# Kernel tuning notes

Measured on AMD Instinct MI355X. Metric: run time of the kernel, lower is better.

## Reference

```python
import jax, jax.numpy as jnp
import numpy as np
import math

N, B, S = 2048, 4, 1024
SFZ, IFZ, H, A = 384, 256, 8, 64
LN_EPS = 1e-5


def setup_inputs() -> dict:
    key = jax.random.key(0)
    ks = jax.random.split(key, 12)
    x = jax.random.normal(ks[0], (N, IFZ), dtype=jnp.float32)
    emb = jax.random.normal(ks[1], (B, S, SFZ), dtype=jnp.float32)
    mask = jax.random.randint(ks[2], (B, S), 0, 2).astype(bool)
    batch = jnp.sort(jax.random.randint(ks[3], (N,), 0, B)).astype(jnp.int64)
    sc = 1.0 / math.sqrt(IFZ)
    scs = 1.0 / math.sqrt(SFZ)
    Wq = jax.random.normal(ks[4], (IFZ, H * A), dtype=jnp.float32) * sc
    Wk = jax.random.normal(ks[5], (SFZ, H * A), dtype=jnp.float32) * scs
    Wv = jax.random.normal(ks[6], (SFZ, H * A), dtype=jnp.float32) * scs
    Wg = jax.random.normal(ks[7], (IFZ, H * A), dtype=jnp.float32) * sc
    bg = jnp.zeros((H * A,), dtype=jnp.float32)
    Wback = jax.random.normal(ks[8], (H * A, IFZ), dtype=jnp.float32) / math.sqrt(H * A)
    bback = jnp.zeros((IFZ,), dtype=jnp.float32)
    gamma = jnp.ones((IFZ,), dtype=jnp.float32)
    beta = jnp.zeros((IFZ,), dtype=jnp.float32)
    return {"x": x, "packed_sequence_emb": emb, "packed_sequence_mask": mask,
            "batch": batch, "Wq": Wq, "Wk": Wk, "Wv": Wv, "Wg": Wg, "bg": bg,
            "Wback": Wback, "bback": bback, "gamma": gamma, "beta": beta}


def _masked_softmax(scores, mask):
    # scores: [N,S,H], mask: [N,S,1] bool; softmax over S with padded entries zeroed
    neg = jnp.finfo(scores.dtype).min
    s = jnp.where(mask, scores, neg)
    s = s - jnp.max(s, axis=1, keepdims=True)
    e = jnp.exp(s) * mask
    return e / (jnp.sum(e, axis=1, keepdims=True) + 1e-9)


def reference(x, packed_sequence_emb, packed_sequence_mask, batch,
              Wq, Wk, Wv, Wg, bg, Wback, bback, gamma, beta):
    scale = math.sqrt(A)
    q = (x @ Wq).reshape(N, H, A)                               # [N,H,A]
    k = (packed_sequence_emb @ Wk).reshape(B, S, H, A)          # [B,S,H,A]
    v = (packed_sequence_emb @ Wv).reshape(B, S, H, A)
    # scores per (node, candidate-batch), then gather node's own batch entry;
    # avoids materializing k[batch] of shape [N,S,H,A]
    scores_all = jnp.einsum('nha,bsha->nbsh', q, k) / scale     # [N,B,S,H]
    idx = batch[:, None, None, None].astype(jnp.int32)
    scores = jnp.take_along_axis(scores_all, idx, axis=1)[:, 0]  # [N,S,H]
    bmask = packed_sequence_mask[batch][..., None]               # [N,S,1]
    w = _masked_softmax(scores, bmask)                           # [N,S,H]
    feat_all = jnp.einsum('nsh,bsha->nbha', w, v)                # [N,B,H,A]
    feat = jnp.take_along_axis(feat_all, idx, axis=1)[:, 0]      # [N,H,A]
    gate = jax.nn.sigmoid(x @ Wg + bg).reshape(N, H, A)
    new = (gate * feat).reshape(N, H * A) @ Wback + bback        # [N,IFZ]
    y = math.sqrt(2.0) * x + new
    mu = jnp.mean(y, axis=-1, keepdims=True)
    var = jnp.mean((y - mu) ** 2, axis=-1, keepdims=True)
    out = (y - mu) * jax.lax.rsqrt(var + LN_EPS) * gamma + beta
    seq_aa_logits = jnp.sum(scores[..., :2], axis=-1)            # [N,S]
    return out, seq_aa_logits
```

## Files before the change

kernel.cpp:

```cpp
#include <hip/hip_runtime.h>
#include <hip/hip_bf16.h>

#define NND 2048
#define BBATCH 4
#define SS 1024
#define SFZ 384
#define IFZ 256
#define HH 8
#define AA 64
#define HA 512
#define NBX 48
#define NSPL 8

typedef __attribute__((ext_vector_type(8))) short bf16x8;
typedef __attribute__((ext_vector_type(4))) float f32x4;

__device__ __forceinline__ unsigned short f2bf(float f) {
    union { float f; unsigned u; } a; a.f = f;
    unsigned r = a.u + 0x7fffu + ((a.u >> 16) & 1u);
    return (unsigned short)(r >> 16);
}
__device__ __forceinline__ float bf2f(unsigned short u) {
    return __uint_as_float((unsigned)u << 16);
}

__device__ __forceinline__ bf16x8 cvt8(const float* __restrict__ p) {
    const float4 f0 = *(const float4*)p;
    const float4 f1 = *(const float4*)(p + 4);
    bf16x8 o;
    o[0] = (short)f2bf(f0.x); o[1] = (short)f2bf(f0.y);
    o[2] = (short)f2bf(f0.z); o[3] = (short)f2bf(f0.w);
    o[4] = (short)f2bf(f1.x); o[5] = (short)f2bf(f1.y);
    o[6] = (short)f2bf(f1.z); o[7] = (short)f2bf(f1.w);
    return o;
}

__device__ __forceinline__ void tile_transpose_h(
    const float* __restrict__ src, unsigned short* __restrict__ dst,
    int K, int N, int kt, int nt, int half, int t)
{
    __shared__ unsigned short tile[32][65];
    const int k0 = kt * 64 + half * 32, n0 = nt * 64;
    const int tr = t >> 6, tc = t & 63;
    #pragma unroll
    for (int r = 0; r < 8; ++r)
        tile[tr + r*4][tc] = f2bf(src[(size_t)(k0 + tr + r*4) * N + n0 + tc]);
    __syncthreads();
    const int rr = t >> 5, cc = t & 31;
    #pragma unroll
    for (int r2 = 0; r2 < 8; ++r2)
        dst[(size_t)(n0 + rr + r2*8) * K + k0 + cc] = tile[cc][rr + r2*8];
}

__global__ __launch_bounds__(256) void prep_kernel(
    const float* __restrict__ Wk, const float* __restrict__ Wv,
    const float* __restrict__ Wq, const float* __restrict__ Wg,
    const float* __restrict__ Wback,
    const void* __restrict__ mask_raw, const void* __restrict__ batch_raw,
    unsigned short* __restrict__ WkT, unsigned short* __restrict__ WvT,
    unsigned short* __restrict__ WqT, unsigned short* __restrict__ WgT,
    unsigned short* __restrict__ WbackT,
    float* __restrict__ mask_f, int* __restrict__ seg)
{
    const int bx = blockIdx.x, t = threadIdx.x;
    if (bx < 384) {
        const int ht = bx >> 1, half = bx & 1;
        if (ht < 48)       tile_transpose_h(Wk, WkT, SFZ, HA, ht/8, ht%8, half, t);
        else if (ht < 96)  { const int i = ht-48;  tile_transpose_h(Wv, WvT, SFZ, HA, i/8, i%8, half, t); }
        else if (ht < 128) { const int i = ht-96;  tile_transpose_h(Wq, WqT, IFZ, HA, i/8, i%8, half, t); }
        else if (ht < 160) { const int i = ht-128; tile_transpose_h(Wg, WgT, IFZ, HA, i/8, i%8, half, t); }
        else               { const int i = ht-160; tile_transpose_h(Wback, WbackT, HA, IFZ, i/4, i%4, half, t); }
        return;
    }
    __shared__ int fl[4];
    __shared__ int fb;
    __shared__ int cnt[4];
    if (t < 4) { fl[t] = 0; cnt[t] = 0; }
    if (t == 0) fb = 0;
    __syncthreads();
    const unsigned char*  mb = (const unsigned char*)mask_raw;
    const unsigned short* mh = (const unsigned short*)mask_raw;
    const unsigned int*   mw = (const unsigned int*)mask_raw;
    int f0 = 0, f1 = 0, f2 = 0, f3 = 0;
    for (int i = t; i < 2048; i += 256) {
        unsigned short h = mh[i];
        if (h == 0x3f80u) f0 = 1;
        if ((i & 1) == 0 && h != 0) f1 = 1;
    }
    for (int i = t; i < 4096; i += 256)
        if ((i & 3) != 0 && mb[i] != 0) f2 = 1;
    for (int i = t; i < 1024; i += 256)
        if ((i & 1) != 0 && mw[i] != 0) f3 = 1;
    const int* bw = (const int*)batch_raw;
    int f4 = 0;
    for (int i = t + 1; i < 2048; i += 256)
        if (bw[i] < bw[i-1]) f4 = 1;
    if (f0) atomicOr(&fl[0], 1);
    if (f1) atomicOr(&fl[1], 1);
    if (f2) atomicOr(&fl[2], 1);
    if (f3) atomicOr(&fl[3], 1);
    if (f4) atomicOr(&fb, 1);
    __syncthreads();
    int mode;
    if (fl[0])      mode = fl[1] ? 1 : 0;
    else if (fl[2]) mode = 2;
    else if (fl[3]) mode = 3;
    else            mode = 4;
    for (int s = t; s < BBATCH*SS; s += 256) {
        int m;
        switch (mode) {
            case 0:  m = (mw[s]   != 0); break;
            case 1:  m = (mh[s]   != 0); break;
            case 2:  m = (mb[s]   != 0); break;
            case 3:  m = (mw[s]   != 0); break;
            default: m = (mw[2*s] != 0); break;
        }
        mask_f[s] = m ? 1.0f : 0.0f;
    }
    const int b64 = fb;
    for (int i = t; i < NND; i += 256) {
        const int bv = (b64 ? bw[2*i] : bw[i]) & 3;
        atomicAdd(&cnt[bv], 1);
    }
    __syncthreads();
    if (t == 0) {
        int s = 0;
        for (int b = 0; b < 4; ++b) { seg[2*b] = s; s += cnt[b]; seg[2*b+1] = s; }
    }
}

__global__ __launch_bounds__(256) void proj_mfma(
    const float* __restrict__ emb, const float* __restrict__ x,
    const unsigned short* __restrict__ WkT, const unsigned short* __restrict__ WvT,
    const unsigned short* __restrict__ WqT, const unsigned short* __restrict__ WgT,
    const float* __restrict__ bg,
    unsigned short* __restrict__ k_blk, unsigned short* __restrict__ vT_bf,
    unsigned short* __restrict__ q_bf, unsigned short* __restrict__ gate_bf)
{
    __shared__ unsigned short v_l[16][520];
    const int t = threadIdx.x, w = t >> 6, lane = t & 63;
    const int m16 = lane & 15, quad = lane >> 4;
    const int bx = blockIdx.x;
    if (bx < 512) {
        const int r0 = (bx >> 1) * 16;
        const int b = r0 >> 10, srow = r0 & (SS - 1);
        const float* ap = emb + (size_t)(r0 + m16) * SFZ + quad * 8;
        bf16x8 af[12];
        #pragma unroll
        for (int j = 0; j < 12; ++j) af[j] = cvt8(ap + j * 32);
        if ((bx & 1) == 0) {
            #pragma unroll
            for (int nt = 0; nt < 8; ++nt) {
                const int n0 = w * 128 + nt * 16;
                const unsigned short* bp = WkT + (size_t)(n0 + m16) * SFZ + quad * 8;
                f32x4 d = (f32x4){0.f, 0.f, 0.f, 0.f};
                #pragma unroll
                for (int j = 0; j < 12; ++j)
                    d = __builtin_amdgcn_mfma_f32_16x16x32_bf16(af[j], *(const bf16x8*)(bp + j * 32), d, 0, 0, 0);
                const int head = n0 >> 6, coff = (n0 & 63) + m16;
                unsigned short* kb = k_blk + (((size_t)(b * HH + head)) * SS) * 64 + coff;
                #pragma unroll
                for (int r = 0; r < 4; ++r)
                    kb[(size_t)(srow + quad * 4 + r) * 64] = f2bf(d[r]);
            }
        } else {
            #pragma unroll
            for (int nt = 0; nt < 8; ++nt) {
                const int n0 = w * 128 + nt * 16;
                const unsigned short* bp = WvT + (size_t)(n0 + m16) * SFZ + quad * 8;
                f32x4 d = (f32x4){0.f, 0.f, 0.f, 0.f};
                #pragma unroll
                for (int j = 0; j < 12; ++j)
                    d = __builtin_amdgcn_mfma_f32_16x16x32_bf16(af[j], *(const bf16x8*)(bp + j * 32), d, 0, 0, 0);
                #pragma unroll
                for (int r = 0; r < 4; ++r)
                    v_l[quad * 4 + r][n0 + m16] = f2bf(d[r]);
            }
            __syncthreads();
            for (int c = t; c < HA; c += 256) {
                unsigned short tmp[16];
                #pragma unroll
                for (int s = 0; s < 16; ++s) tmp[s] = v_l[s][c];
                unsigned short* dst = vT_bf + ((size_t)b * HA + c) * SS + srow;
                *(uint4*)dst       = ((const uint4*)tmp)[0];
                *(uint4*)(dst + 8) = ((const uint4*)tmp)[1];
            }
        }
    } else {
        const int i = bx - 512;
        const int r0 = (i >> 2) * 16;
        const int tensor = (i & 3) >> 1, half = i & 1;
        const unsigned short* Wt = tensor ? WgT : WqT;
        const float* ap = x + (size_t)(r0 + m16) * IFZ + quad * 8;
        bf16x8 af[8];
        #pragma unroll
        for (int j = 0; j < 8; ++j) af[j] = cvt8(ap + j * 32);
        #pragma unroll
        for (int nt = 0; nt < 4; ++nt) {
            const int n0 = half * 256 + w * 64 + nt * 16;
            const unsigned short* bp = Wt + (size_t)(n0 + m16) * IFZ + quad * 8;
            f32x4 d = (f32x4){0.f, 0.f, 0.f, 0.f};
            #pragma unroll
            for (int j = 0; j < 8; ++j)
                d = __builtin_amdgcn_mfma_f32_16x16x32_bf16(af[j], *(const bf16x8*)(bp + j * 32), d, 0, 0, 0);
            if (tensor == 0) {
                #pragma unroll
                for (int r = 0; r < 4; ++r)
                    q_bf[(size_t)(r0 + quad * 4 + r) * HA + n0 + m16] = f2bf(d[r]);
            } else {
                const float bgv = bg[n0 + m16];
                #pragma unroll
                for (int r = 0; r < 4; ++r)
                    gate_bf[(size_t)(r0 + quad * 4 + r) * HA + n0 + m16] =
                        f2bf(1.f / (1.f + __expf(-(d[r] + bgv))));
            }
        }
    }
}

__global__ __launch_bounds__(256) void attn_kernel(
    const unsigned short* __restrict__ k_blk, const unsigned short* __restrict__ vT_bf,
    const unsigned short* __restrict__ q_bf, const float* __restrict__ mask_f,
    const int* __restrict__ seg, unsigned short* __restrict__ part_O,
    float2* __restrict__ part_ml, float* __restrict__ out_logits)
{
    __shared__ unsigned short P_lds[4][16][136];
    __shared__ float raw[2][16][132];
    const int bid = blockIdx.x;
    const int xcd = bid & 7;
    const int b   = xcd >> 1;
    const int idx = (bid >> 3) * 2 + (xcd & 1);
    const int z    = idx & 15;
    const int xblk = idx >> 4;
    const int hz    = z >> 3;
    const int split = z & 7;
    const int n0 = seg[2*b] + xblk * 16;
    const int nend = seg[2*b + 1];
    if (n0 >= nend) return;
    const int nvalid = min(16, nend - n0);

    const int t = threadIdx.x;
    const int w = t >> 6, lane = t & 63;
    const int m16 = lane & 15, quad = lane >> 4;
    const int h = hz * 4 + w;
    const int s0 = split * 128;

    int nq = n0 + m16; if (nq >= nend) nq = nend - 1;
    const unsigned short* qp = q_bf + (size_t)nq * HA + h * AA + quad * 8;
    const bf16x8 qa0 = *(const bf16x8*)qp;
    const bf16x8 qa1 = *(const bf16x8*)(qp + 32);

    const unsigned short* kb = k_blk + ((size_t)(b * HH + h)) * SS * 64;
    const unsigned short* vb = vT_bf + ((size_t)b * HA + h * AA) * SS;
    unsigned short (*Pw)[136] = P_lds[w];

    float msk[8];
    #pragma unroll
    for (int st = 0; st < 8; ++st)
        msk[st] = mask_f[b * SS + s0 + st * 16 + m16];

    f32x4 d[8];
    #pragma unroll
    for (int st = 0; st < 8; ++st) {
        const unsigned short* kp = kb + (size_t)(s0 + st * 16 + m16) * 64 + quad * 8;
        const bf16x8 b0 = *(const bf16x8*)kp;
        const bf16x8 b1 = *(const bf16x8*)(kp + 32);
        f32x4 acc = (f32x4){0.f, 0.f, 0.f, 0.f};
        acc = __builtin_amdgcn_mfma_f32_16x16x32_bf16(qa0, b0, acc, 0, 0, 0);
        acc = __builtin_amdgcn_mfma_f32_16x16x32_bf16(qa1, b1, acc, 0, 0, 0);
        #pragma unroll
        for (int r = 0; r < 4; ++r) acc[r] *= 0.125f;
        d[st] = acc;
    }
    if (hz == 0) {
        if (w < 2) {
            #pragma unroll
            for (int st = 0; st < 8; ++st)
                #pragma unroll
                for (int r = 0; r < 4; ++r)
                    raw[w][quad * 4 + r][st * 16 + m16] = d[st][r];
        }
        __syncthreads();
        for (int i = t; i < 16 * 128; i += 256) {
            const int node = i >> 7, sp = i & 127;
            if (node < nvalid)
                out_logits[(size_t)(n0 + node) * SS + s0 + sp] =
                    raw[0][node][sp] + raw[1][node][sp];
        }
    }
    float m_s[4], l_s[4];
    #pragma unroll
    for (int r = 0; r < 4; ++r) {
        float mx = -3.0e38f;
        #pragma unroll
        for (int st = 0; st < 8; ++st)
            mx = (msk[st] > 0.5f) ? fmaxf(mx, d[st][r]) : mx;
        mx = fmaxf(mx, __shfl_xor(mx, 1));
        mx = fmaxf(mx, __shfl_xor(mx, 2));
        mx = fmaxf(mx, __shfl_xor(mx, 4));
        mx = fmaxf(mx, __shfl_xor(mx, 8));
        m_s[r] = mx;
        float cs = 0.f;
        #pragma unroll
        for (int st = 0; st < 8; ++st) {
            const float e = (msk[st] > 0.5f) ? __expf(d[st][r] - mx) : 0.f;
            d[st][r] = e;
            cs += e;
        }
        cs += __shfl_xor(cs, 1);
        cs += __shfl_xor(cs, 2);
        cs += __shfl_xor(cs, 4);
        cs += __shfl_xor(cs, 8);
        l_s[r] = cs;
    }
    #pragma unroll
    for (int st = 0; st < 8; ++st)
        #pragma unroll
        for (int r = 0; r < 4; ++r)
            Pw[quad * 4 + r][st * 16 + m16] = f2bf(d[st][r]);
    f32x4 facc[4];
    #pragma unroll
    for (int a = 0; a < 4; ++a) facc[a] = (f32x4){0.f, 0.f, 0.f, 0.f};
    #pragma unroll
    for (int sub = 0; sub < 4; ++sub) {
        const bf16x8 pa = *(const bf16x8*)&Pw[m16][sub * 32 + quad * 8];
        const unsigned short* vp0 = vb + (size_t)m16 * SS + s0 + sub * 32 + quad * 8;
        #pragma unroll
        for (int a = 0; a < 4; ++a) {
            const bf16x8 vfr = *(const bf16x8*)(vp0 + (size_t)(a * 16) * SS);
            facc[a] = __builtin_amdgcn_mfma_f32_16x16x32_bf16(pa, vfr, facc[a], 0, 0, 0);
        }
    }
    unsigned short* po = part_O + (size_t)split * NND * HA;
    #pragma unroll
    for (int a = 0; a < 4; ++a)
        #pragma unroll
        for (int r = 0; r < 4; ++r) {
            const int row = quad * 4 + r;
            if (row < nvalid)
                po[(size_t)(n0 + row) * HA + h * AA + a * 16 + m16] = f2bf(facc[a][r]);
        }
    if (m16 == 0) {
        #pragma unroll
        for (int r = 0; r < 4; ++r) {
            const int row = quad * 4 + r;
            if (row < nvalid)
                part_ml[(size_t)split * NND * HH + (size_t)(n0 + row) * HH + h] =
                    make_float2(m_s[r], l_s[r]);
        }
    }
}

__global__ __launch_bounds__(256) void back_ln_fused(
    const unsigned short* __restrict__ part_O, const float2* __restrict__ part_ml,
    const unsigned short* __restrict__ gate_bf, const unsigned short* __restrict__ WbackT,
    const float* __restrict__ x, const float* __restrict__ bback,
    const float* __restrict__ gamma, const float* __restrict__ beta,
    float* __restrict__ out)
{
    __shared__ float coef[NSPL][4][8];
    __shared__ unsigned short gf_l[4][520];
    __shared__ float nl[4][260];
    const int t = threadIdx.x, w = t >> 6, lane = t & 63;
    const int m16 = lane & 15, quad = lane >> 4;
    const int r0 = blockIdx.x * 4;
    if (t < 32) {
        const int row = t >> 3, h = t & 7, n = r0 + row;
        float2 ml[NSPL];
        #pragma unroll
        for (int s = 0; s < NSPL; ++s)
            ml[s] = part_ml[(size_t)s * NND * HH + (size_t)n * HH + h];
        float M = -3.0e38f;
        #pragma unroll
        for (int s = 0; s < NSPL; ++s) M = fmaxf(M, ml[s].x);
        float L = 0.f;
        float e[NSPL];
        #pragma unroll
        for (int s = 0; s < NSPL; ++s) { e[s] = __expf(ml[s].x - M); L += ml[s].y * e[s]; }
        const float invL = 1.f / (L + 1e-9f);
        #pragma unroll
        for (int s = 0; s < NSPL; ++s) coef[s][row][h] = e[s] * invL;
    }
    __syncthreads();
    #pragma unroll
    for (int it = 0; it < 2; ++it) {
        const int i = (t + it * 256) * 4;
        const int row = i >> 9, c = i & (HA - 1), h = c >> 6;
        const int n = r0 + row;
        float4 o = make_float4(0.f, 0.f, 0.f, 0.f);
        #pragma unroll
        for (int s = 0; s < NSPL; ++s) {
            const ushort4 p = *(const ushort4*)&part_O[(size_t)s * NND * HA + (size_t)n * HA + c];
            const float cf = coef[s][row][h];
            o.x = fmaf(bf2f(p.x), cf, o.x); o.y = fmaf(bf2f(p.y), cf, o.y);
            o.z = fmaf(bf2f(p.z), cf, o.z); o.w = fmaf(bf2f(p.w), cf, o.w);
        }
        const ushort4 g = *(const ushort4*)&gate_bf[(size_t)n * HA + c];
        ushort4 ob;
        ob.x = f2bf(bf2f(g.x) * o.x); ob.y = f2bf(bf2f(g.y) * o.y);
        ob.z = f2bf(bf2f(g.z) * o.z); ob.w = f2bf(bf2f(g.w) * o.w);
        *(ushort4*)&gf_l[row][c] = ob;
    }
    __syncthreads();
    bf16x8 af[16];
    #pragma unroll
    for (int j = 0; j < 16; ++j)
        af[j] = *(const bf16x8*)&gf_l[m16 & 3][quad * 8 + j * 32];
    #pragma unroll
    for (int nt = 0; nt < 4; ++nt) {
        const int n0 = w * 64 + nt * 16;
        const unsigned short* bp = WbackT + (size_t)(n0 + m16) * HA + quad * 8;
        f32x4 d = (f32x4){0.f, 0.f, 0.f, 0.f};
        #pragma unroll
        for (int j = 0; j < 16; ++j)
            d = __builtin_amdgcn_mfma_f32_16x16x32_bf16(af[j], *(const bf16x8*)(bp + j * 32), d, 0, 0, 0);
        const float bb = bback[n0 + m16];
        #pragma unroll
        for (int r = 0; r < 4; ++r) {
            const int rr = quad * 4 + r;
            if (rr < 4) nl[rr][n0 + m16] = d[r] + bb;
        }
    }
    __syncthreads();
    const int row = t >> 6, li = t & 63;
    const float* xr = x + (size_t)(r0 + row) * IFZ;
    float yv[4];
    float s1 = 0.f, s2 = 0.f;
    #pragma unroll
    for (int j = 0; j < 4; ++j) {
        const int c = li + j * 64;
        const float v = fmaf(1.41421356237309515f, xr[c], nl[row][c]);
        yv[j] = v; s1 += v; s2 += v * v;
    }
    #pragma unroll
    for (int off = 32; off >= 1; off >>= 1) {
        s1 += __shfl_xor(s1, off);
        s2 += __shfl_xor(s2, off);
    }
    const float mu  = s1 * (1.f / IFZ);
    const float var = s2 * (1.f / IFZ) - mu * mu;
    const float rv  = rsqrtf(var + 1e-5f);
    float* orow = out + (size_t)(r0 + row) * IFZ;
    #pragma unroll
    for (int j = 0; j < 4; ++j) {
        const int c = li + j * 64;
        orow[c] = (yv[j] - mu) * rv * gamma[c] + beta[c];
    }
}

extern "C" void kernel_launch(void* const* d_in, const int* in_sizes, int n_in,
                              void* d_out, int out_size, void* d_ws, size_t ws_size,
                              hipStream_t stream) {
    const float* x     = (const float*)d_in[0];
    const float* emb   = (const float*)d_in[1];
    const void*  mraw  = d_in[2];
    const void*  braw  = d_in[3];
    const float* Wq    = (const float*)d_in[4];
    const float* Wk    = (const float*)d_in[5];
    const float* Wv    = (const float*)d_in[6];
    const float* Wg    = (const float*)d_in[7];
    const float* bg    = (const float*)d_in[8];
    const float* Wback = (const float*)d_in[9];
    const float* bback = (const float*)d_in[10];
    const float* gamma = (const float*)d_in[11];
    const float* beta  = (const float*)d_in[12];

    char* ws = (char*)d_ws;
    const size_t MB = 1048576;
    size_t off = 0;
    float*          mask_f  = (float*)(ws + off);  off += 16384;
    int*            seg     = (int*)(ws + off);    off += 16384;
    unsigned short* WkT     = (unsigned short*)(ws + off); off += 393216;
    unsigned short* WvT     = (unsigned short*)(ws + off); off += 393216;
    unsigned short* WqT     = (unsigned short*)(ws + off); off += 262144;
    unsigned short* WgT     = (unsigned short*)(ws + off); off += 262144;
    unsigned short* WbackT  = (unsigned short*)(ws + off); off += 262144;
    unsigned short* k_blk   = (unsigned short*)(ws + off); off += 4*MB;
    unsigned short* vT_bf   = (unsigned short*)(ws + off); off += 4*MB;
    unsigned short* q_bf    = (unsigned short*)(ws + off); off += 2*MB;
    unsigned short* gate_bf = (unsigned short*)(ws + off); off += 2*MB;
    unsigned short* part_O  = (unsigned short*)(ws + off); off += 16*MB;
    float2*         part_ml = (float2*)(ws + off); off += 1*MB;

    float* out        = (float*)d_out;
    float* out_logits = out + (size_t)NND * IFZ;

    hipLaunchKernelGGL(prep_kernel, dim3(385), dim3(256), 0, stream,
                       Wk, Wv, Wq, Wg, Wback, mraw, braw,
                       WkT, WvT, WqT, WgT, WbackT, mask_f, seg);
    hipLaunchKernelGGL(proj_mfma, dim3(1024), dim3(256), 0, stream,
                       emb, x, WkT, WvT, WqT, WgT, bg, k_blk, vT_bf, q_bf, gate_bf);
    hipLaunchKernelGGL(attn_kernel, dim3(BBATCH * NBX * 16), dim3(256), 0, stream,
                       k_blk, vT_bf, q_bf, mask_f, seg, part_O, part_ml, out_logits);
    hipLaunchKernelGGL(back_ln_fused, dim3(NND / 4), dim3(256), 0, stream,
                       part_O, part_ml, gate_bf, WbackT, x, bback, gamma, beta, out);
}
```

Measured before the change: 202.4 us.

## Drop weight-transpose prep kernel and gather fp32 weights directly in MFMA loops

Removes the separate prep kernel that transposed and converted the weight matrices to bf16. The projection and back-projection kernels now read fp32 weights with strided gathers and convert them inline. Mask and segment preparation moves into an extra block of the projection kernel, saving one launch and the intermediate weight buffers. The cost is strided, uncoalesced fp32 weight loads and repeated conversion in every block, which may slow the GEMM inner loops.

```diff
diff --git a/kernel.cpp b/kernel.cpp
--- a/kernel.cpp
+++ b/kernel.cpp
@@ -35,109 +35,28 @@
     return o;
 }
 
-__device__ __forceinline__ void tile_transpose_h(
-    const float* __restrict__ src, unsigned short* __restrict__ dst,
-    int K, int N, int kt, int nt, int half, int t)
-{
-    __shared__ unsigned short tile[32][65];
-    const int k0 = kt * 64 + half * 32, n0 = nt * 64;
-    const int tr = t >> 6, tc = t & 63;
-    #pragma unroll
-    for (int r = 0; r < 8; ++r)
-        tile[tr + r*4][tc] = f2bf(src[(size_t)(k0 + tr + r*4) * N + n0 + tc]);
-    __syncthreads();
-    const int rr = t >> 5, cc = t & 31;
-    #pragma unroll
-    for (int r2 = 0; r2 < 8; ++r2)
-        dst[(size_t)(n0 + rr + r2*8) * K + k0 + cc] = tile[cc][rr + r2*8];
-}
-
-__global__ __launch_bounds__(256) void prep_kernel(
+__device__ __forceinline__ bf16x8 gatherB(const float* __restrict__ wj) {
+    bf16x8 o;
+    #pragma unroll
+    for (int e = 0; e < 8; ++e)
+        o[e] = (short)f2bf(wj[(size_t)e * HA]);
+    return o;
+}
+
+__global__ __launch_bounds__(256) void proj_mfma(
+    const float* __restrict__ emb, const float* __restrict__ x,
     const float* __restrict__ Wk, const float* __restrict__ Wv,
     const float* __restrict__ Wq, const float* __restrict__ Wg,
-    const float* __restrict__ Wback,
+    const float* __restrict__ bg,
     const void* __restrict__ mask_raw, const void* __restrict__ batch_raw,
-    unsigned short* __restrict__ WkT, unsigned short* __restrict__ WvT,
-    unsigned short* __restrict__ WqT, unsigned short* __restrict__ WgT,
-    unsigned short* __restrict__ WbackT,
+    unsigned short* __restrict__ k_blk, unsigned short* __restrict__ vT_bf,
+    unsigned short* __restrict__ q_bf, unsigned short* __restrict__ gate_bf,
     float* __restrict__ mask_f, int* __restrict__ seg)
 {
-    const int bx = blockIdx.x, t = threadIdx.x;
-    if (bx < 384) {
-        const int ht = bx >> 1, half = bx & 1;
-        if (ht < 48)       tile_transpose_h(Wk, WkT, SFZ, HA, ht/8, ht%8, half, t);
-        else if (ht < 96)  { const int i = ht-48;  tile_transpose_h(Wv, WvT, SFZ, HA, i/8, i%8, half, t); }
-        else if (ht < 128) { const int i = ht-96;  tile_transpose_h(Wq, WqT, IFZ, HA, i/8, i%8, half, t); }
-        else if (ht < 160) { const int i = ht-128; tile_transpose_h(Wg, WgT, IFZ, HA, i/8, i%8, half, t); }
-        else               { const int i = ht-160; tile_transpose_h(Wback, WbackT, HA, IFZ, i/4, i%4, half, t); }
-        return;
-    }
+    __shared__ unsigned short v_l[16][520];
     __shared__ int fl[4];
     __shared__ int fb;
     __shared__ int cnt[4];
-    if (t < 4) { fl[t] = 0; cnt[t] = 0; }
-    if (t == 0) fb = 0;
-    __syncthreads();
-    const unsigned char*  mb = (const unsigned char*)mask_raw;
-    const unsigned short* mh = (const unsigned short*)mask_raw;
-    const unsigned int*   mw = (const unsigned int*)mask_raw;
-    int f0 = 0, f1 = 0, f2 = 0, f3 = 0;
-    for (int i = t; i < 2048; i += 256) {
-        unsigned short h = mh[i];
-        if (h == 0x3f80u) f0 = 1;
-        if ((i & 1) == 0 && h != 0) f1 = 1;
-    }
-    for (int i = t; i < 4096; i += 256)
-        if ((i & 3) != 0 && mb[i] != 0) f2 = 1;
-    for (int i = t; i < 1024; i += 256)
-        if ((i & 1) != 0 && mw[i] != 0) f3 = 1;
-    const int* bw = (const int*)batch_raw;
-    int f4 = 0;
-    for (int i = t + 1; i < 2048; i += 256)
-        if (bw[i] < bw[i-1]) f4 = 1;
-    if (f0) atomicOr(&fl[0], 1);
-    if (f1) atomicOr(&fl[1], 1);
-    if (f2) atomicOr(&fl[2], 1);
-    if (f3) atomicOr(&fl[3], 1);
-    if (f4) atomicOr(&fb, 1);
-    __syncthreads();
-    int mode;
-    if (fl[0])      mode = fl[1] ? 1 : 0;
-    else if (fl[2]) mode = 2;
-    else if (fl[3]) mode = 3;
-    else            mode = 4;
-    for (int s = t; s < BBATCH*SS; s += 256) {
-        int m;
-        switch (mode) {
-            case 0:  m = (mw[s]   != 0); break;
-            case 1:  m = (mh[s]   != 0); break;
-            case 2:  m = (mb[s]   != 0); break;
-            case 3:  m = (mw[s]   != 0); break;
-            default: m = (mw[2*s] != 0); break;
-        }
-        mask_f[s] = m ? 1.0f : 0.0f;
-    }
-    const int b64 = fb;
-    for (int i = t; i < NND; i += 256) {
-        const int bv = (b64 ? bw[2*i] : bw[i]) & 3;
-        atomicAdd(&cnt[bv], 1);
-    }
-    __syncthreads();
-    if (t == 0) {
-        int s = 0;
-        for (int b = 0; b < 4; ++b) { seg[2*b] = s; s += cnt[b]; seg[2*b+1] = s; }
-    }
-}
-
-__global__ __launch_bounds__(256) void proj_mfma(
-    const float* __restrict__ emb, const float* __restrict__ x,
-    const unsigned short* __restrict__ WkT, const unsigned short* __restrict__ WvT,
-    const unsigned short* __restrict__ WqT, const unsigned short* __restrict__ WgT,
-    const float* __restrict__ bg,
-    unsigned short* __restrict__ k_blk, unsigned short* __restrict__ vT_bf,
-    unsigned short* __restrict__ q_bf, unsigned short* __restrict__ gate_bf)
-{
-    __shared__ unsigned short v_l[16][520];
     const int t = threadIdx.x, w = t >> 6, lane = t & 63;
     const int m16 = lane & 15, quad = lane >> 4;
     const int bx = blockIdx.x;
@@ -152,11 +71,12 @@
             #pragma unroll
             for (int nt = 0; nt < 8; ++nt) {
                 const int n0 = w * 128 + nt * 16;
-                const unsigned short* bp = WkT + (size_t)(n0 + m16) * SFZ + quad * 8;
+                const float* wp = Wk + (size_t)(quad * 8) * HA + n0 + m16;
                 f32x4 d = (f32x4){0.f, 0.f, 0.f, 0.f};
                 #pragma unroll
                 for (int j = 0; j < 12; ++j)
-                    d = __builtin_amdgcn_mfma_f32_16x16x32_bf16(af[j], *(const bf16x8*)(bp + j * 32), d, 0, 0, 0);
+                    d = __builtin_amdgcn_mfma_f32_16x16x32_bf16(
+                        af[j], gatherB(wp + (size_t)j * 32 * HA), d, 0, 0, 0);
                 const int head = n0 >> 6, coff = (n0 & 63) + m16;
                 unsigned short* kb = k_blk + (((size_t)(b * HH + head)) * SS) * 64 + coff;
                 #pragma unroll
@@ -167,11 +87,12 @@
             #pragma unroll
             for (int nt = 0; nt < 8; ++nt) {
                 const int n0 = w * 128 + nt * 16;
-                const unsigned short* bp = WvT + (size_t)(n0 + m16) * SFZ + quad * 8;
+                const float* wp = Wv + (size_t)(quad * 8) * HA + n0 + m16;
                 f32x4 d = (f32x4){0.f, 0.f, 0.f, 0.f};
                 #pragma unroll
                 for (int j = 0; j < 12; ++j)
-                    d = __builtin_amdgcn_mfma_f32_16x16x32_bf16(af[j], *(const bf16x8*)(bp + j * 32), d, 0, 0, 0);
+                    d = __builtin_amdgcn_mfma_f32_16x16x32_bf16(
+                        af[j], gatherB(wp + (size_t)j * 32 * HA), d, 0, 0, 0);
                 #pragma unroll
                 for (int r = 0; r < 4; ++r)
                     v_l[quad * 4 + r][n0 + m16] = f2bf(d[r]);
@@ -186,11 +107,11 @@
                 *(uint4*)(dst + 8) = ((const uint4*)tmp)[1];
             }
         }
-    } else {
+    } else if (bx < 1024) {
         const int i = bx - 512;
         const int r0 = (i >> 2) * 16;
         const int tensor = (i & 3) >> 1, half = i & 1;
-        const unsigned short* Wt = tensor ? WgT : WqT;
+        const float* Wt = tensor ? Wg : Wq;
         const float* ap = x + (size_t)(r0 + m16) * IFZ + quad * 8;
         bf16x8 af[8];
         #pragma unroll
@@ -198,11 +119,12 @@
         #pragma unroll
         for (int nt = 0; nt < 4; ++nt) {
             const int n0 = half * 256 + w * 64 + nt * 16;
-            const unsigned short* bp = Wt + (size_t)(n0 + m16) * IFZ + quad * 8;
+            const float* wp = Wt + (size_t)(quad * 8) * HA + n0 + m16;
             f32x4 d = (f32x4){0.f, 0.f, 0.f, 0.f};
             #pragma unroll
             for (int j = 0; j < 8; ++j)
-                d = __builtin_amdgcn_mfma_f32_16x16x32_bf16(af[j], *(const bf16x8*)(bp + j * 32), d, 0, 0, 0);
+                d = __builtin_amdgcn_mfma_f32_16x16x32_bf16(
+                    af[j], gatherB(wp + (size_t)j * 32 * HA), d, 0, 0, 0);
             if (tensor == 0) {
                 #pragma unroll
                 for (int r = 0; r < 4; ++r)
@@ -214,6 +136,59 @@
                     gate_bf[(size_t)(r0 + quad * 4 + r) * HA + n0 + m16] =
                         f2bf(1.f / (1.f + __expf(-(d[r] + bgv))));
             }
+        }
+    } else {
+        if (t < 4) { fl[t] = 0; cnt[t] = 0; }
+        if (t == 0) fb = 0;
+        __syncthreads();
+        const unsigned char*  mb = (const unsigned char*)mask_raw;
+        const unsigned short* mh = (const unsigned short*)mask_raw;
+        const unsigned int*   mw = (const unsigned int*)mask_raw;
+        int f0 = 0, f1 = 0, f2 = 0, f3 = 0;
+        for (int i = t; i < 2048; i += 256) {
+            unsigned short h = mh[i];
+            if (h == 0x3f80u) f0 = 1;
+            if ((i & 1) == 0 && h != 0) f1 = 1;
+        }
+        for (int i = t; i < 4096; i += 256)
+            if ((i & 3) != 0 && mb[i] != 0) f2 = 1;
+        for (int i = t; i < 1024; i += 256)
+            if ((i & 1) != 0 && mw[i] != 0) f3 = 1;
+        const int* bw = (const int*)batch_raw;
+        int f4 = 0;
+        for (int i = t + 1; i < 2048; i += 256)
+            if (bw[i] < bw[i-1]) f4 = 1;
+        if (f0) atomicOr(&fl[0], 1);
+        if (f1) atomicOr(&fl[1], 1);
+        if (f2) atomicOr(&fl[2], 1);
+        if (f3) atomicOr(&fl[3], 1);
+        if (f4) atomicOr(&fb, 1);
+        __syncthreads();
+        int mode;
+        if (fl[0])      mode = fl[1] ? 1 : 0;
+        else if (fl[2]) mode = 2;
+        else if (fl[3]) mode = 3;
+        else            mode = 4;
+        for (int s = t; s < BBATCH*SS; s += 256) {
+            int m;
+            switch (mode) {
+                case 0:  m = (mw[s]   != 0); break;
+                case 1:  m = (mh[s]   != 0); break;
+                case 2:  m = (mb[s]   != 0); break;
+                case 3:  m = (mw[s]   != 0); break;
+                default: m = (mw[2*s] != 0); break;
+            }
+            mask_f[s] = m ? 1.0f : 0.0f;
+        }
+        const int b64 = fb;
+        for (int i = t; i < NND; i += 256) {
+            const int bv = (b64 ? bw[2*i] : bw[i]) & 3;
+            atomicAdd(&cnt[bv], 1);
+        }
+        __syncthreads();
+        if (t == 0) {
+            int s = 0;
+            for (int b = 0; b < 4; ++b) { seg[2*b] = s; s += cnt[b]; seg[2*b+1] = s; }
         }
     }
 }
@@ -353,7 +328,7 @@
 
 __global__ __launch_bounds__(256) void back_ln_fused(
     const unsigned short* __restrict__ part_O, const float2* __restrict__ part_ml,
-    const unsigned short* __restrict__ gate_bf, const unsigned short* __restrict__ WbackT,
+    const unsigned short* __restrict__ gate_bf, const float* __restrict__ Wback,
     const float* __restrict__ x, const float* __restrict__ bback,
     const float* __restrict__ gamma, const float* __restrict__ beta,
     float* __restrict__ out)
@@ -409,11 +384,17 @@
     #pragma unroll
     for (int nt = 0; nt < 4; ++nt) {
         const int n0 = w * 64 + nt * 16;
-        const unsigned short* bp = WbackT + (size_t)(n0 + m16) * HA + quad * 8;
+        const float* wp = Wback + (size_t)(quad * 8) * IFZ + n0 + m16;
         f32x4 d = (f32x4){0.f, 0.f, 0.f, 0.f};
         #pragma unroll
-        for (int j = 0; j < 16; ++j)
-            d = __builtin_amdgcn_mfma_f32_16x16x32_bf16(af[j], *(const bf16x8*)(bp + j * 32), d, 0, 0, 0);
+        for (int j = 0; j < 16; ++j) {
+            const float* wj = wp + (size_t)j * 32 * IFZ;
+            bf16x8 bfr;
+            #pragma unroll
+            for (int e = 0; e < 8; ++e)
+                bfr[e] = (short)f2bf(wj[(size_t)e * IFZ]);
+            d = __builtin_amdgcn_mfma_f32_16x16x32_bf16(af[j], bfr, d, 0, 0, 0);
+        }
         const float bb = bback[n0 + m16];
         #pragma unroll
         for (int r = 0; r < 4; ++r) {
@@ -470,11 +451,6 @@
     size_t off = 0;
     float*          mask_f  = (float*)(ws + off);  off += 16384;
     int*            seg     = (int*)(ws + off);    off += 16384;
-    unsigned short* WkT     = (unsigned short*)(ws + off); off += 393216;
-    unsigned short* WvT     = (unsigned short*)(ws + off); off += 393216;
-    unsigned short* WqT     = (unsigned short*)(ws + off); off += 262144;
-    unsigned short* WgT     = (unsigned short*)(ws + off); off += 262144;
-    unsigned short* WbackT  = (unsigned short*)(ws + off); off += 262144;
     unsigned short* k_blk   = (unsigned short*)(ws + off); off += 4*MB;
     unsigned short* vT_bf   = (unsigned short*)(ws + off); off += 4*MB;
     unsigned short* q_bf    = (unsigned short*)(ws + off); off += 2*MB;
@@ -485,13 +461,11 @@
     float* out        = (float*)d_out;
     float* out_logits = out + (size_t)NND * IFZ;
 
-    hipLaunchKernelGGL(prep_kernel, dim3(385), dim3(256), 0, stream,
-                       Wk, Wv, Wq, Wg, Wback, mraw, braw,
-                       WkT, WvT, WqT, WgT, WbackT, mask_f, seg);
-    hipLaunchKernelGGL(proj_mfma, dim3(1024), dim3(256), 0, stream,
-                       emb, x, WkT, WvT, WqT, WgT, bg, k_blk, vT_bf, q_bf, gate_bf);
+    hipLaunchKernelGGL(proj_mfma, dim3(1025), dim3(256), 0, stream,
+                       emb, x, Wk, Wv, Wq, Wg, bg, mraw, braw,
+                       k_blk, vT_bf, q_bf, gate_bf, mask_f, seg);
     hipLaunchKernelGGL(attn_kernel, dim3(BBATCH * NBX * 16), dim3(256), 0, stream,
                        k_blk, vT_bf, q_bf, mask_f, seg, part_O, part_ml, out_logits);
     hipLaunchKernelGGL(back_ln_fused, dim3(NND / 4), dim3(256), 0, stream,
-                       part_O, part_ml, gate_bf, WbackT, x, bback, gamma, beta, out);
-}
+                       part_O, part_ml, gate_bf, Wback, x, bback, gamma, beta, out);
+}
```

After: 243.3 us. +20.2%, slower.
